# Performance work log

Measured on AMD Instinct MI355X. Metric: run time of the kernel, lower is better.

The kernel has to match this reference:

```python
import jax, jax.numpy as jnp
import numpy as np

N_NODES = 100000
N_EDGES = 300000
D_IN = 256
D_OUT = 256


def setup_inputs() -> dict:
    key = jax.random.key(0)
    k1, k2, k3 = jax.random.split(key, 3)
    z = jax.random.normal(k1, (N_NODES, D_IN), dtype=jnp.float32)
    edge_index = jax.random.randint(k2, (2, N_EDGES), 0, N_NODES, dtype=jnp.int64)
    # Linear(input_dim, out_dim): weight [out, in], stored transposed for x @ W
    W = jax.random.normal(k3, (D_IN, D_OUT), dtype=jnp.float32) / np.sqrt(D_IN)
    b = jnp.zeros((D_OUT,), dtype=jnp.float32)
    return {"z": z, "edge_index": edge_index, "W": W, "b": b}


def reference(z, edge_index, W, b):
    # h = Linear(z): [N, D_out]
    h = z @ W + b
    # gather endpoint embeddings and take per-edge dot product
    src = h[edge_index[0]]  # [E, D_out]
    dst = h[edge_index[1]]  # [E, D_out]
    value = jnp.sum(src * dst, axis=1)  # [E]
    return jax.nn.sigmoid(value)
```

## Files before the change

### kernel.cpp

```cpp
#include <hip/hip_runtime.h>
#include <hip/hip_bf16.h>
#include <hip/hip_fp16.h>
#include <math.h>


#define D_DIM 256
#define NBLK 256

typedef __attribute__((ext_vector_type(8))) _Float16 half8;
typedef __attribute__((ext_vector_type(4))) _Float16 half4;
typedef __attribute__((ext_vector_type(4))) float f32x4;

__device__ half8 g_Wf[8 * 256 * 4];

__global__ __launch_bounds__(256) void pack_w_kernel(const float* __restrict__ W) {
  int t = blockIdx.x * 256 + threadIdx.x;
  int kb = t >> 10;
  int qd = (t >> 8) & 3;
  int n  = t & 255;
  int fn = n >> 4;
  int fr = n & 15;
  half8 o;
#pragma unroll
  for (int j = 0; j < 8; j++)
    o[j] = (_Float16)W[(size_t)(kb * 32 + qd * 8 + j) * D_DIM + n];
  g_Wf[kb * 1024 + fn * 64 + qd * 16 + fr] = o;
}

__device__ inline void stage_write(char* tile, int tid, float4 A, float4 B) {
  int row = tid >> 6;
  int inner = (tid & 63) * 8;
  int sw = (row & 7) << 4;
  half4 p0, p1;
  p0[0] = (_Float16)A.x; p0[1] = (_Float16)A.y;
  p0[2] = (_Float16)A.z; p0[3] = (_Float16)A.w;
  p1[0] = (_Float16)B.x; p1[1] = (_Float16)B.y;
  p1[2] = (_Float16)B.z; p1[3] = (_Float16)B.w;
  *(half4*)(tile + row * 512 + (inner ^ sw)) = p0;
  *(half4*)(tile + (row + 8) * 512 + (inner ^ sw)) = p1;
}

__global__ __launch_bounds__(512) void gemm_mfma_kernel(
    const float* __restrict__ z, const float* __restrict__ b,
    __half* __restrict__ h, int nrows) {
  __shared__ char smem[147456];
  const int tid = threadIdx.x;
  const int lane = tid & 63;
  const int wv = tid >> 6;
  const int fr = lane & 15;
  const int qd = lane >> 4;

  {
    const char* gsrc = (const char*)g_Wf;
#pragma unroll
    for (int rnd = 0; rnd < 16; rnd++) {
      int off = rnd * 8192 + wv * 1024;
      __builtin_amdgcn_global_load_lds(
          (const __attribute__((address_space(1))) void*)(gsrc + off + lane * 16),
          (__attribute__((address_space(3))) void*)(smem + off),
          16, 0, 0);
    }
  }
  float bias0 = b[wv * 32 + fr];
  float bias1 = b[wv * 32 + 16 + fr];

  char* atile0 = smem + 131072;
  char* atile1 = smem + 139264;
  const char* zb = (const char*)z;
  const int nstrips = (nrows + 15) >> 4;

  int s0 = blockIdx.x;
  float4 ld0, ld1;
  {
    const char* sb = zb + (size_t)s0 * 16384;
    ld0 = *(const float4*)(sb + tid * 16);
    ld1 = *(const float4*)(sb + 8192 + tid * 16);
  }
  stage_write(atile0, tid, ld0, ld1);
  __syncthreads();

  const half8* bw = (const half8*)smem;
  int cur = 0;

#pragma unroll 1
  for (int s = s0; s < nstrips; s += NBLK) {
    char* at = cur ? atile1 : atile0;
    char* an = cur ? atile0 : atile1;
    const bool hasnext = (s + NBLK) < nstrips;

    if (hasnext) {
      const char* sb = zb + (size_t)(s + NBLK) * 16384;
      ld0 = *(const float4*)(sb + tid * 16);
      ld1 = *(const float4*)(sb + 8192 + tid * 16);
    }
    asm volatile("" ::: "memory");

    f32x4 acc0 = (f32x4)0.f, acc1 = (f32x4)0.f;
    const char* abase = at + fr * 512;
    const int sw = (fr & 7) << 4;
#pragma unroll
    for (int kb = 0; kb < 8; kb++) {
      half8 af = *(const half8*)(abase + ((kb * 64 + qd * 16) ^ sw));
      half8 bf0 = bw[kb * 1024 + (2 * wv) * 64 + lane];
      half8 bf1 = bw[kb * 1024 + (2 * wv + 1) * 64 + lane];
      acc0 = __builtin_amdgcn_mfma_f32_16x16x32_f16(af, bf0, acc0, 0, 0, 0);
      acc1 = __builtin_amdgcn_mfma_f32_16x16x32_f16(af, bf1, acc1, 0, 0, 0);
    }
    __syncthreads();

    __half* et = (__half*)(at + wv * 1024);
#pragma unroll
    for (int r = 0; r < 4; r++) {
      et[(qd * 4 + r) * 32 + fr]      = __float2half(acc0[r] + bias0);
      et[(qd * 4 + r) * 32 + 16 + fr] = __float2half(acc1[r] + bias1);
    }
    int row = lane >> 2, c = lane & 3;
    float4 v = *(const float4*)((const char*)et + row * 64 + c * 16);

    if (hasnext) stage_write(an, tid, ld0, ld1);

    int grow = s * 16 + row;
    if (grow < nrows)
      *(float4*)((char*)h + (size_t)grow * 512 + wv * 64 + c * 16) = v;

    cur ^= 1;
    __syncthreads();
  }
}

__global__ __launch_bounds__(256) void edge_dot_kernel(
    const int* __restrict__ ei, const __half* __restrict__ h,
    float* __restrict__ out, int E) {
  int wid = (blockIdx.x * blockDim.x + threadIdx.x) >> 6;
  int lane = threadIdx.x & 63;
  int ebase = wid * 8;
  if (ebase >= E) return;
  const int half = lane >> 5;
  const int off = lane & 31;

  float4 v[8];
#pragma unroll
  for (int q = 0; q < 8; q++) {
    int e = ebase + q;
    e = e < E ? e : (E - 1);
    int node = half ? ei[E + e] : ei[e];
    v[q] = *(const float4*)((const __half*)h + (size_t)node * D_DIM + off * 8);
  }

  float res = 0.f;
#pragma unroll
  for (int q = 0; q < 8; q++) {
    float4 w;
    w.x = __shfl_xor(v[q].x, 32);
    w.y = __shfl_xor(v[q].y, 32);
    w.z = __shfl_xor(v[q].z, 32);
    w.w = __shfl_xor(v[q].w, 32);
    const __half2* a2 = (const __half2*)&v[q];
    const __half2* b2 = (const __half2*)&w;
    float part = 0.f;
#pragma unroll
    for (int j = 0; j < 4; j++) {
      float2 fa = __half22float2(a2[j]);
      float2 fb = __half22float2(b2[j]);
      part += fa.x * fb.x + fa.y * fb.y;
    }
#pragma unroll
    for (int m = 1; m <= 16; m <<= 1) part += __shfl_xor(part, m);
    res = (lane == q) ? part : res;
  }
  if (lane < 8) {
    int e = ebase + lane;
    if (e < E) out[e] = 1.0f / (1.0f + __expf(-res));
  }
}

extern "C" void kernel_launch(void* const* d_in, const int* in_sizes, int n_in,
                              void* d_out, int out_size, void* d_ws, size_t ws_size,
                              hipStream_t stream) {
  const float* z  = (const float*)d_in[0];
  const int*   ei = (const int*)d_in[1];
  const float* W  = (const float*)d_in[2];
  const float* b  = (const float*)d_in[3];
  float* out = (float*)d_out;
  __half* h  = (__half*)d_ws;

  const int nnodes = in_sizes[0] / D_DIM;
  const int E = in_sizes[1] / 2;

  pack_w_kernel<<<32, 256, 0, stream>>>(W);

  gemm_mfma_kernel<<<NBLK, 512, 0, stream>>>(z, b, h, nnodes);

  int waves = (E + 7) / 8;
  dim3 grid_edge(((size_t)waves * 64 + 255) / 256);
  edge_dot_kernel<<<grid_edge, 256, 0, stream>>>(ei, h, out, E);
}
```

Measured before the change: 202.4 us.

## Deepen GEMM prefetch to two strips ahead and write full contiguous rows

```diff
diff --git a/kernel.cpp b/kernel.cpp
--- a/kernel.cpp
+++ b/kernel.cpp
@@ -40,6 +40,56 @@
   *(half4*)(tile + (row + 8) * 512 + (inner ^ sw)) = p1;
 }
 
+#define SYNC_LDS() do {                                        \
+    asm volatile("" ::: "memory");                             \
+    asm volatile("s_waitcnt lgkmcnt(0)" ::: "memory");         \
+    __builtin_amdgcn_s_barrier();                              \
+    asm volatile("" ::: "memory");                             \
+  } while (0)
+
+#define BODY(S, AT, AN, LC0, LC1, LN0, LN1) do {               \
+    if ((S) + 2 * NBLK < nstrips) {                            \
+      const char* sb = zb + (size_t)((S) + 2 * NBLK) * 16384;  \
+      LN0 = *(const float4*)(sb + tid * 16);                   \
+      LN1 = *(const float4*)(sb + 8192 + tid * 16);            \
+    }                                                          \
+    asm volatile("" ::: "memory");                             \
+    f32x4 acc0 = (f32x4)0.f, acc1 = (f32x4)0.f;                \
+    {                                                          \
+      const char* abase = (AT) + fr * 512;                     \
+      const int swz = (fr & 7) << 4;                           \
+      _Pragma("unroll")                                        \
+      for (int kb = 0; kb < 8; kb++) {                         \
+        half8 af = *(const half8*)(abase + ((kb * 64 + qd * 16) ^ swz)); \
+        half8 bf0 = bw[kb * 1024 + (2 * wv) * 64 + lane];      \
+        half8 bf1 = bw[kb * 1024 + (2 * wv + 1) * 64 + lane];  \
+        acc0 = __builtin_amdgcn_mfma_f32_16x16x32_f16(af, bf0, acc0, 0, 0, 0); \
+        acc1 = __builtin_amdgcn_mfma_f32_16x16x32_f16(af, bf1, acc1, 0, 0, 0); \
+      }                                                        \
+    }                                                          \
+    SYNC_LDS();                 \
+    {                                                          \
+      char* tp = (char*)(AT);                                  \
+      _Pragma("unroll")                                        \
+      for (int r = 0; r < 4; r++) {                            \
+        int row = qd * 4 + r;                                  \
+        int rs = (row & 7) << 4;                               \
+        *(__half*)(tp + row * 512 + ((wv * 64 + 2 * fr) ^ rs)) =       \
+            __float2half(acc0[r] + bias0);                     \
+        *(__half*)(tp + row * 512 + ((wv * 64 + 32 + 2 * fr) ^ rs)) =  \
+            __float2half(acc1[r] + bias1);                     \
+      }                                                        \
+    }                                                          \
+    if ((S) + NBLK < nstrips) stage_write((AN), tid, LC0, LC1);\
+    SYNC_LDS();        \
+    {                                                          \
+      int row = tid >> 5;                                      \
+      int byo = (tid & 31) * 16;                               \
+      float4 v = *(const float4*)((AT) + row * 512 + (byo ^ ((row & 7) << 4))); \
+      *(float4*)((char*)h + (size_t)(S) * 8192 + tid * 16) = v;\
+    }                                                          \
+  } while (0)
+
 __global__ __launch_bounds__(512) void gemm_mfma_kernel(
     const float* __restrict__ z, const float* __restrict__ b,
     __half* __restrict__ h, int nrows) {
@@ -61,70 +111,37 @@
           16, 0, 0);
     }
   }
-  float bias0 = b[wv * 32 + fr];
-  float bias1 = b[wv * 32 + 16 + fr];
+  const float bias0 = b[wv * 32 + fr];
+  const float bias1 = b[wv * 32 + 16 + fr];
 
   char* atile0 = smem + 131072;
   char* atile1 = smem + 139264;
   const char* zb = (const char*)z;
   const int nstrips = (nrows + 15) >> 4;
-
-  int s0 = blockIdx.x;
-  float4 ld0, ld1;
+  const half8* bw = (const half8*)smem;
+
+  const int s0 = blockIdx.x;
   {
     const char* sb = zb + (size_t)s0 * 16384;
-    ld0 = *(const float4*)(sb + tid * 16);
-    ld1 = *(const float4*)(sb + 8192 + tid * 16);
-  }
-  stage_write(atile0, tid, ld0, ld1);
+    float4 p0 = *(const float4*)(sb + tid * 16);
+    float4 p1 = *(const float4*)(sb + 8192 + tid * 16);
+    stage_write(atile0, tid, p0, p1);
+  }
   __syncthreads();
 
-  const half8* bw = (const half8*)smem;
-  int cur = 0;
-
-#pragma unroll 1
-  for (int s = s0; s < nstrips; s += NBLK) {
-    char* at = cur ? atile1 : atile0;
-    char* an = cur ? atile0 : atile1;
-    const bool hasnext = (s + NBLK) < nstrips;
-
-    if (hasnext) {
-      const char* sb = zb + (size_t)(s + NBLK) * 16384;
-      ld0 = *(const float4*)(sb + tid * 16);
-      ld1 = *(const float4*)(sb + 8192 + tid * 16);
-    }
-    asm volatile("" ::: "memory");
-
-    f32x4 acc0 = (f32x4)0.f, acc1 = (f32x4)0.f;
-    const char* abase = at + fr * 512;
-    const int sw = (fr & 7) << 4;
-#pragma unroll
-    for (int kb = 0; kb < 8; kb++) {
-      half8 af = *(const half8*)(abase + ((kb * 64 + qd * 16) ^ sw));
-      half8 bf0 = bw[kb * 1024 + (2 * wv) * 64 + lane];
-      half8 bf1 = bw[kb * 1024 + (2 * wv + 1) * 64 + lane];
-      acc0 = __builtin_amdgcn_mfma_f32_16x16x32_f16(af, bf0, acc0, 0, 0, 0);
-      acc1 = __builtin_amdgcn_mfma_f32_16x16x32_f16(af, bf1, acc1, 0, 0, 0);
-    }
-    __syncthreads();
-
-    __half* et = (__half*)(at + wv * 1024);
-#pragma unroll
-    for (int r = 0; r < 4; r++) {
-      et[(qd * 4 + r) * 32 + fr]      = __float2half(acc0[r] + bias0);
-      et[(qd * 4 + r) * 32 + 16 + fr] = __float2half(acc1[r] + bias1);
-    }
-    int row = lane >> 2, c = lane & 3;
-    float4 v = *(const float4*)((const char*)et + row * 64 + c * 16);
-
-    if (hasnext) stage_write(an, tid, ld0, ld1);
-
-    int grow = s * 16 + row;
-    if (grow < nrows)
-      *(float4*)((char*)h + (size_t)grow * 512 + wv * 64 + c * 16) = v;
-
-    cur ^= 1;
-    __syncthreads();
+  float4 lA0, lA1, lB0, lB1;
+  if (s0 + NBLK < nstrips) {
+    const char* sb = zb + (size_t)(s0 + NBLK) * 16384;
+    lA0 = *(const float4*)(sb + tid * 16);
+    lA1 = *(const float4*)(sb + 8192 + tid * 16);
+  }
+
+  int s = s0;
+  while (true) {
+    BODY(s, atile0, atile1, lA0, lA1, lB0, lB1);
+    s += NBLK; if (s >= nstrips) break;
+    BODY(s, atile1, atile0, lB0, lB1, lA0, lA1);
+    s += NBLK; if (s >= nstrips) break;
   }
 }
 
```

After: 206.5 us. 2.0% more time.
